# Kernel tuning notes

Hardware: AMD Instinct MI355X
Metric: run time of the kernel (lower is better)

Reference implementation:

```python
import jax, jax.numpy as jnp
import numpy as np

L, H, D, E, V, MAXS = 12, 12, 64, 768, 50257, 1024

def _ln(x, g, b, eps=1e-5):
    m = jnp.mean(x, axis=-1, keepdims=True)
    v = jnp.mean(jnp.square(x - m), axis=-1, keepdims=True)
    return (x - m) * jax.lax.rsqrt(v + eps) * g + b

def setup_inputs() -> dict:
    key = jax.random.key(0)
    ks = jax.random.split(key, 16)
    s = 0.02
    inp = {
        "input_ids": jax.random.randint(ks[0], (1, 1), 0, V),
        "past_key": jax.random.normal(ks[1], (L, 1, H, MAXS, D), jnp.float32),
        "past_value": jax.random.normal(ks[2], (L, 1, H, MAXS, D), jnp.float32),
        "past_seq_len": 1023,
        "attention_mask": jnp.ones((1, MAXS), jnp.float32),
        "wte": jax.random.normal(ks[3], (V, E), jnp.float32) * s,
        "wpe": jax.random.normal(ks[4], (MAXS, E), jnp.float32) * s,
        "ln1_g": jnp.ones((L, E), jnp.float32),
        "ln1_b": jnp.zeros((L, E), jnp.float32),
        "attn_w": jax.random.normal(ks[5], (L, E, 3 * E), jnp.float32) * s,
        "attn_b": jnp.zeros((L, 3 * E), jnp.float32),
        "proj_w": jax.random.normal(ks[6], (L, E, E), jnp.float32) * s,
        "proj_b": jnp.zeros((L, E), jnp.float32),
        "ln2_g": jnp.ones((L, E), jnp.float32),
        "ln2_b": jnp.zeros((L, E), jnp.float32),
        "fc_w": jax.random.normal(ks[7], (L, E, 4 * E), jnp.float32) * s,
        "fc_b": jnp.zeros((L, 4 * E), jnp.float32),
        "mlp_w": jax.random.normal(ks[8], (L, 4 * E, E), jnp.float32) * s,
        "mlp_b": jnp.zeros((L, E), jnp.float32),
        "lnf_g": jnp.ones((E,), jnp.float32),
        "lnf_b": jnp.zeros((E,), jnp.float32),
    }
    return inp

def reference(input_ids, past_key, past_value, past_seq_len, attention_mask,
              wte, wpe, ln1_g, ln1_b, attn_w, attn_b, proj_w, proj_b,
              ln2_g, ln2_b, fc_w, fc_b, mlp_w, mlp_b, lnf_g, lnf_b):
    S = int(past_seq_len)  # static cache length
    h = wte[input_ids] + wpe[S]                      # [1,1,E]
    bias = (1.0 - attention_mask[:, :S + 1]) * -1e9  # [1,S+1]
    scale = 1.0 / jnp.sqrt(jnp.float32(D))
    pk, pv = past_key, past_value
    for l in range(L):
        x = _ln(h, ln1_g[l], ln1_b[l])
        qkv = x @ attn_w[l] + attn_b[l]              # [1,1,3E]
        q, k, v = jnp.split(qkv, 3, axis=-1)
        q = q.reshape(1, 1, H, D).transpose(0, 2, 1, 3)  # [1,H,1,D]
        k = k.reshape(1, 1, H, D).transpose(0, 2, 1, 3)
        v = v.reshape(1, 1, H, D).transpose(0, 2, 1, 3)
        k_full = jnp.concatenate([pk[l, :, :, :S, :], k], axis=2)  # [1,H,S+1,D]
        v_full = jnp.concatenate([pv[l, :, :, :S, :], v], axis=2)
        scores = jnp.einsum('bhqd,bhkd->bhqk', q, k_full) * scale
        scores = scores + bias[:, None, None, :]
        attn = jax.nn.softmax(scores, axis=-1)
        o = jnp.einsum('bhqk,bhkd->bhqd', attn, v_full)
        o = o.transpose(0, 2, 1, 3).reshape(1, 1, H * D)
        h = h + o @ proj_w[l] + proj_b[l]
        x2 = _ln(h, ln2_g[l], ln2_b[l])
        h = h + jax.nn.gelu(x2 @ fc_w[l] + fc_b[l], approximate=True) @ mlp_w[l] + mlp_b[l]
        pk = pk.at[l, :, :, S, :].set(k[:, :, 0, :])
        pv = pv.at[l, :, :, S, :].set(v[:, :, 0, :])
    h = _ln(h, lnf_g, lnf_b)
    logits = h @ wte.T                               # [1,1,V] (tied lm_head)
    return (logits, pk, pv)
```

## Files before the change

kernel.cpp:

```cpp
#include <hip/hip_runtime.h>
#include <math.h>

#define EMB 768
#define NH 12
#define HD 64
#define NL 12
#define NV 50257
#define MAXS 1024
#define S_PAST 1023
#define E3 2304
#define E4 3072

#define WS_H    0
#define WS_QKV  768
#define WS_FC   3072
#define WS_PART 6144

__device__ __forceinline__ void blockReduce2(float& a, float& b, volatile float* ra, volatile float* rb) {
  int lane = threadIdx.x & 63, wid = threadIdx.x >> 6;
#pragma unroll
  for (int o = 32; o > 0; o >>= 1) { a += __shfl_down(a, o); b += __shfl_down(b, o); }
  if (lane == 0) { ra[wid] = a; rb[wid] = b; }
  __syncthreads();
  if (threadIdx.x == 0) {
    ra[0] = ra[0] + ra[1] + ra[2] + ra[3];
    rb[0] = rb[0] + rb[1] + rb[2] + rb[3];
  }
  __syncthreads();
  a = ra[0]; b = rb[0];
}

__global__ void copy_embed(const float* __restrict__ pk, const float* __restrict__ pv,
                           float* __restrict__ opk, float* __restrict__ opv,
                           const int* __restrict__ ids, const float* __restrict__ wte,
                           const float* __restrict__ wpe, const float* __restrict__ attn_b,
                           float* __restrict__ hvec, float* __restrict__ qkv) {
  int tid = threadIdx.x;
  if (blockIdx.x >= 2048) {
    int bi = blockIdx.x - 2048;
    qkv[bi * 256 + tid] = attn_b[bi * 256 + tid];
    if (bi < 3) {
      int id = ids[0];
      int e = bi * 256 + tid;
      hvec[e] = wte[(size_t)id * EMB + e] + wpe[(size_t)S_PAST * EMB + e];
    }
    return;
  }
  const size_t n4 = (size_t)NL * NH * MAXS * HD / 4;
  const float4* pk4 = (const float4*)pk;
  const float4* pv4 = (const float4*)pv;
  float4* opk4 = (float4*)opk;
  float4* opv4 = (float4*)opv;
  for (size_t i = (size_t)blockIdx.x * 256 + tid; i < n4; i += (size_t)2048 * 256) {
    opk4[i] = pk4[i];
    opv4[i] = pv4[i];
  }
}

template<int R>
__global__ void ln_gemv4(const float* __restrict__ hvec, const float* __restrict__ g,
                         const float* __restrict__ bb, const float* __restrict__ W,
                         float* __restrict__ out, int N, int l) {
  __shared__ float lh[EMB];
  __shared__ float xs[R];
  __shared__ float ra[4], rb[4];
  __shared__ float4 red[4][64];
  int tid = threadIdx.x, lane = tid & 63, wid = tid >> 6;
  float s1 = 0.f, s2 = 0.f;
  for (int e = tid; e < EMB; e += 256) { float v = hvec[e]; lh[e] = v; s1 += v; s2 += v * v; }
  blockReduce2(s1, s2, ra, rb);
  float mean = s1 * (1.f / EMB);
  float var = s2 * (1.f / EMB) - mean * mean;
  float rstd = rsqrtf(var + 1e-5f);
  int e0 = blockIdx.y * R;
  if (tid < R) {
    int e = e0 + tid;
    xs[tid] = (lh[e] - mean) * rstd * g[l * EMB + e] + bb[l * EMB + e];
  }
  __syncthreads();
  int j4 = blockIdx.x * 64 + lane;
  int N4 = N >> 2;
  const float4* p = (const float4*)(W + (size_t)l * EMB * N) + (size_t)e0 * N4 + j4 + (size_t)wid * N4;
  float4 w[R / 4];
#pragma unroll
  for (int i = 0; i < R / 4; i++) w[i] = p[(size_t)(i * 4) * N4];
  float4 acc = {0.f, 0.f, 0.f, 0.f};
#pragma unroll
  for (int i = 0; i < R / 4; i++) {
    float x = xs[wid + i * 4];
    acc.x += x * w[i].x; acc.y += x * w[i].y; acc.z += x * w[i].z; acc.w += x * w[i].w;
  }
  red[wid][lane] = acc;
  __syncthreads();
  if (wid == 0) {
    float4 a0 = red[0][lane], a1 = red[1][lane], a2 = red[2][lane], a3 = red[3][lane];
    float rx = a0.x + a1.x + a2.x + a3.x;
    float ry = a0.y + a1.y + a2.y + a3.y;
    float rz = a0.z + a1.z + a2.z + a3.z;
    float rw = a0.w + a1.w + a2.w + a3.w;
    float* op = out + (size_t)j4 * 4;
    atomicAdd(op + 0, rx); atomicAdd(op + 1, ry);
    atomicAdd(op + 2, rz); atomicAdd(op + 3, rw);
  }
}

__global__ void attn_kv(const float* __restrict__ qkv, const float* __restrict__ pk,
                        const float* __restrict__ pv, const float* __restrict__ mask,
                        float* __restrict__ opk, float* __restrict__ opv,
                        float* __restrict__ part, int l) {
  int h = blockIdx.x >> 4, c = blockIdx.x & 15;
  int tid = threadIdx.x, lane = tid & 63, wid = tid >> 6;
  int sub = tid & 15, grp = tid >> 4;
  __shared__ float4 qs4[16];
  __shared__ float sc[64];
  __shared__ float4 redo[4][16];
  if (tid < 16) qs4[tid] = ((const float4*)(qkv + h * 64))[tid];
  __syncthreads();
  size_t base = ((size_t)(l * NH + h) * MAXS) * HD;
  const float4* K4 = (const float4*)(pk + base);
  const float4* V4 = (const float4*)(pv + base);
  int t0 = c * 64;
  float4 kreg[4];
#pragma unroll
  for (int i = 0; i < 4; i++) {
    int t = t0 + grp + i * 16;
    kreg[i] = (t == S_PAST) ? ((const float4*)(qkv + EMB + h * 64))[sub] : K4[(size_t)t * 16 + sub];
  }
  if (c == 15 && grp == 15)
    ((float4*)(opk + base))[(size_t)S_PAST * 16 + sub] = kreg[3];
  float4 q4 = qs4[sub];
#pragma unroll
  for (int i = 0; i < 4; i++) {
    int key = grp + i * 16;
    float p = q4.x * kreg[i].x + q4.y * kreg[i].y + q4.z * kreg[i].z + q4.w * kreg[i].w;
    p += __shfl_xor(p, 1); p += __shfl_xor(p, 2);
    p += __shfl_xor(p, 4); p += __shfl_xor(p, 8);
    if (sub == 0) sc[key] = p * 0.125f + (1.f - mask[t0 + key]) * (-1e9f);
  }
  __syncthreads();
  if (wid == 0) {
    float a = sc[lane];
    float m = a;
#pragma unroll
    for (int o = 32; o > 0; o >>= 1) m = fmaxf(m, __shfl_down(m, o));
    m = __shfl(m, 0);
    float ea = expf(a - m);
    sc[lane] = ea;
    float s = ea;
#pragma unroll
    for (int o = 32; o > 0; o >>= 1) s += __shfl_down(s, o);
    if (lane == 0) { part[(h * 16 + c) * 68 + 0] = m; part[(h * 16 + c) * 68 + 1] = s; }
  }
  __syncthreads();
  float4 vreg[4];
#pragma unroll
  for (int i = 0; i < 4; i++) {
    int t = t0 + grp + i * 16;
    vreg[i] = (t == S_PAST) ? ((const float4*)(qkv + 2 * EMB + h * 64))[sub] : V4[(size_t)t * 16 + sub];
  }
  if (c == 15 && grp == 15)
    ((float4*)(opv + base))[(size_t)S_PAST * 16 + sub] = vreg[3];
  float4 acc = {0.f, 0.f, 0.f, 0.f};
#pragma unroll
  for (int i = 0; i < 4; i++) {
    float w = sc[grp + i * 16];
    acc.x += w * vreg[i].x; acc.y += w * vreg[i].y; acc.z += w * vreg[i].z; acc.w += w * vreg[i].w;
  }
  acc.x += __shfl_xor(acc.x, 16); acc.y += __shfl_xor(acc.y, 16);
  acc.z += __shfl_xor(acc.z, 16); acc.w += __shfl_xor(acc.w, 16);
  acc.x += __shfl_xor(acc.x, 32); acc.y += __shfl_xor(acc.y, 32);
  acc.z += __shfl_xor(acc.z, 32); acc.w += __shfl_xor(acc.w, 32);
  if (lane < 16) redo[wid][lane] = acc;
  __syncthreads();
  if (tid < 16) {
    float4 a0 = redo[0][tid], a1 = redo[1][tid], a2 = redo[2][tid], a3 = redo[3][tid];
    float4 r;
    r.x = a0.x + a1.x + a2.x + a3.x;
    r.y = a0.y + a1.y + a2.y + a3.y;
    r.z = a0.z + a1.z + a2.z + a3.z;
    r.w = a0.w + a1.w + a2.w + a3.w;
    ((float4*)(part + (h * 16 + c) * 68 + 4))[tid] = r;
  }
}

__global__ void proj_attn(const float* __restrict__ part, const float* __restrict__ W,
                          const float* __restrict__ bias, const float* __restrict__ fc_b,
                          float* __restrict__ hout, float* __restrict__ wfc, int l) {
  int jb = blockIdx.x;
  int rt = blockIdx.y;
  int h = rt >> 2, esub = rt & 3;
  int tid = threadIdx.x, lane = tid & 63, wid = tid >> 6;
  __shared__ float xs[16];
  __shared__ float4 red[4][64];
  if (tid < 16) {
    float M = -1e30f;
#pragma unroll
    for (int cc = 0; cc < 16; cc++) M = fmaxf(M, part[(h * 16 + cc) * 68]);
    float T = 0.f, o = 0.f;
    int d = esub * 16 + tid;
#pragma unroll
    for (int cc = 0; cc < 16; cc++) {
      float w = expf(part[(h * 16 + cc) * 68] - M);
      T += part[(h * 16 + cc) * 68 + 1] * w;
      o += part[(h * 16 + cc) * 68 + 4 + d] * w;
    }
    xs[tid] = o / T;
  }
  int bid = rt * 3 + jb;
  if (bid < 12) wfc[bid * 256 + tid] = fc_b[l * E4 + bid * 256 + tid];
  __syncthreads();
  int j4 = jb * 64 + lane;
  const int N4 = EMB >> 2;
  int r0 = h * 64 + esub * 16;
  const float4* p = (const float4*)(W + (size_t)l * EMB * EMB) + (size_t)(r0 + wid) * N4 + j4;
  float4 w[4];
#pragma unroll
  for (int i = 0; i < 4; i++) w[i] = p[(size_t)(i * 4) * N4];
  float4 acc = {0.f, 0.f, 0.f, 0.f};
#pragma unroll
  for (int i = 0; i < 4; i++) {
    float x = xs[wid + i * 4];
    acc.x += x * w[i].x; acc.y += x * w[i].y; acc.z += x * w[i].z; acc.w += x * w[i].w;
  }
  red[wid][lane] = acc;
  __syncthreads();
  if (wid == 0) {
    float4 a0 = red[0][lane], a1 = red[1][lane], a2 = red[2][lane], a3 = red[3][lane];
    float rx = a0.x + a1.x + a2.x + a3.x;
    float ry = a0.y + a1.y + a2.y + a3.y;
    float rz = a0.z + a1.z + a2.z + a3.z;
    float rw = a0.w + a1.w + a2.w + a3.w;
    if (rt == 0) {
      const float* bp = bias + l * EMB + jb * 256 + lane * 4;
      rx += bp[0]; ry += bp[1]; rz += bp[2]; rw += bp[3];
    }
    float* op = hout + (size_t)jb * 256 + (size_t)lane * 4;
    atomicAdd(op + 0, rx); atomicAdd(op + 1, ry);
    atomicAdd(op + 2, rz); atomicAdd(op + 3, rw);
  }
}

__global__ void mlp_gemv4(const float* __restrict__ fcv, const float* __restrict__ W,
                          const float* __restrict__ bias, const float* __restrict__ attn_b,
                          float* __restrict__ hout, float* __restrict__ qkv, int l) {
  __shared__ float xs[64];
  __shared__ float4 red[4][64];
  int tid = threadIdx.x, lane = tid & 63, wid = tid >> 6;
  int e0 = blockIdx.y * 64;
  if (tid < 64) {
    float x = fcv[e0 + tid];
    xs[tid] = 0.5f * x * (1.f + tanhf(0.7978845608028654f * (x + 0.044715f * x * x * x)));
  }
  int bid = blockIdx.y * 3 + blockIdx.x;
  if (l + 1 < NL && bid < 9) qkv[bid * 256 + tid] = attn_b[(l + 1) * E3 + bid * 256 + tid];
  __syncthreads();
  int j4 = blockIdx.x * 64 + lane;
  const int N4 = EMB >> 2;
  const float4* p = (const float4*)(W + (size_t)l * E4 * EMB) + (size_t)(e0 + wid) * N4 + j4;
  float4 w[16];
#pragma unroll
  for (int i = 0; i < 16; i++) w[i] = p[(size_t)(i * 4) * N4];
  float4 acc = {0.f, 0.f, 0.f, 0.f};
#pragma unroll
  for (int i = 0; i < 16; i++) {
    float x = xs[wid + i * 4];
    acc.x += x * w[i].x; acc.y += x * w[i].y; acc.z += x * w[i].z; acc.w += x * w[i].w;
  }
  red[wid][lane] = acc;
  __syncthreads();
  if (wid == 0) {
    float4 a0 = red[0][lane], a1 = red[1][lane], a2 = red[2][lane], a3 = red[3][lane];
    float rx = a0.x + a1.x + a2.x + a3.x;
    float ry = a0.y + a1.y + a2.y + a3.y;
    float rz = a0.z + a1.z + a2.z + a3.z;
    float rw = a0.w + a1.w + a2.w + a3.w;
    if (blockIdx.y == 0) {
      const float* bp = bias + l * EMB + j4 * 4;
      rx += bp[0]; ry += bp[1]; rz += bp[2]; rw += bp[3];
    }
    float* op = hout + (size_t)j4 * 4;
    atomicAdd(op + 0, rx); atomicAdd(op + 1, ry);
    atomicAdd(op + 2, rz); atomicAdd(op + 3, rw);
  }
}

__global__ void logits_lnf(const float* __restrict__ hvec, const float* __restrict__ g,
                           const float* __restrict__ b, const float* __restrict__ wte,
                           float* __restrict__ out) {
  __shared__ float4 xs4[192];
  __shared__ float ra[4], rb[4];
  int tid = threadIdx.x, lane = tid & 63, wid = tid >> 6;
  float s1 = 0.f, s2 = 0.f;
  float v0[3];
  int k = 0;
  for (int e = tid; e < EMB; e += 256, k++) { float v = hvec[e]; v0[k] = v; s1 += v; s2 += v * v; }
  blockReduce2(s1, s2, ra, rb);
  float mean = s1 * (1.f / EMB);
  float var = s2 * (1.f / EMB) - mean * mean;
  float rstd = rsqrtf(var + 1e-5f);
  k = 0;
  for (int e = tid; e < EMB; e += 256, k++)
    ((float*)xs4)[e] = (v0[k] - mean) * rstd * g[e] + b[e];
  __syncthreads();
  int v = blockIdx.x * 4 + wid;
  if (v >= NV) return;
  const float4* row = (const float4*)(wte + (size_t)v * EMB);
  float4 a0 = row[lane], a1 = row[lane + 64], a2 = row[lane + 128];
  float4 x0 = xs4[lane], x1 = xs4[lane + 64], x2 = xs4[lane + 128];
  float acc = a0.x * x0.x + a0.y * x0.y + a0.z * x0.z + a0.w * x0.w
            + a1.x * x1.x + a1.y * x1.y + a1.z * x1.z + a1.w * x1.w
            + a2.x * x2.x + a2.y * x2.y + a2.z * x2.z + a2.w * x2.w;
#pragma unroll
  for (int o = 32; o > 0; o >>= 1) acc += __shfl_down(acc, o);
  if (lane == 0) out[v] = acc;
}

extern "C" void kernel_launch(void* const* d_in, const int* in_sizes, int n_in,
                              void* d_out, int out_size, void* d_ws, size_t ws_size,
                              hipStream_t stream) {
  const int* input_ids = (const int*)d_in[0];
  const float* past_key = (const float*)d_in[1];
  const float* past_value = (const float*)d_in[2];
  const float* mask = (const float*)d_in[4];
  const float* wte = (const float*)d_in[5];
  const float* wpe = (const float*)d_in[6];
  const float* ln1_g = (const float*)d_in[7];
  const float* ln1_b = (const float*)d_in[8];
  const float* attn_w = (const float*)d_in[9];
  const float* attn_b = (const float*)d_in[10];
  const float* proj_w = (const float*)d_in[11];
  const float* proj_b = (const float*)d_in[12];
  const float* ln2_g = (const float*)d_in[13];
  const float* ln2_b = (const float*)d_in[14];
  const float* fc_w = (const float*)d_in[15];
  const float* fc_b = (const float*)d_in[16];
  const float* mlp_w = (const float*)d_in[17];
  const float* mlp_b = (const float*)d_in[18];
  const float* lnf_g = (const float*)d_in[19];
  const float* lnf_b = (const float*)d_in[20];

  float* out = (float*)d_out;
  float* out_logits = out;
  float* out_pk = out + NV;
  float* out_pv = out_pk + (size_t)NL * NH * MAXS * HD;

  float* ws = (float*)d_ws;
  float* wh = ws + WS_H;
  float* wqkv = ws + WS_QKV;
  float* wfc = ws + WS_FC;
  float* wpart = ws + WS_PART;

  copy_embed<<<2057, 256, 0, stream>>>(past_key, past_value, out_pk, out_pv,
                                       input_ids, wte, wpe, attn_b, wh, wqkv);

  for (int l = 0; l < NL; l++) {
    ln_gemv4<32><<<dim3(9, 24), 256, 0, stream>>>(wh, ln1_g, ln1_b, attn_w, wqkv, E3, l);
    attn_kv<<<192, 256, 0, stream>>>(wqkv, past_key, past_value, mask, out_pk, out_pv, wpart, l);
    proj_attn<<<dim3(3, 48), 256, 0, stream>>>(wpart, proj_w, proj_b, fc_b, wh, wfc, l);
    ln_gemv4<32><<<dim3(12, 24), 256, 0, stream>>>(wh, ln2_g, ln2_b, fc_w, wfc, E4, l);
    mlp_gemv4<<<dim3(3, 48), 256, 0, stream>>>(wfc, mlp_w, mlp_b, attn_b, wh, wqkv, l);
  }
  logits_lnf<<<12565, 256, 0, stream>>>(wh, lnf_g, lnf_b, wte, out_logits);
}
```

Before: 498.5 us.

## Fuse per-layer phases with in-kernel flag sync and overlap KV-cache copy in waits

Replaces five launches per layer with two kernels. Inside each kernel, blocks run different phases (QKV gemv, attention, projection, then FC and MLP) and order themselves with global atomic counters and release flags. The upfront bulk copy of the KV cache is removed. Blocks that are waiting on a flag instead take copy tiles from a shared atomic ticket, and the final logits kernel finishes any tiles that remain. The goals are to cut launch overhead and to hide the large cache copy behind dependent work. The risks are spin-wait deadlock if the waiting blocks are not co-resident with the producers, and extra atomic traffic.

```diff
diff --git a/kernel.cpp b/kernel.cpp
--- a/kernel.cpp
+++ b/kernel.cpp
@@ -11,10 +11,71 @@
 #define E3 2304
 #define E4 3072
 
-#define WS_H    0
-#define WS_QKV  768
-#define WS_FC   3072
-#define WS_PART 6144
+typedef unsigned int u32;
+
+#define KV_F4 2359296u
+#define TILE_F4 512u
+#define HALF_TILES 4608u
+#define NTILES 9216u
+
+#define WI_TICKET 0
+#define WI_CNT(l,k) (32 + ((l)*3 + (k)) * 16)
+#define WI_REL(l,k) (1024 + ((l)*3 + (k)) * 16)
+#define WF_H    2048
+#define WF_QKV  (WF_H + EMB)
+#define WF_FC   (WF_QKV + E3)
+#define WF_PART (WF_FC + E4)
+
+struct CopyCtx {
+  const float4* pk4; const float4* pv4;
+  float4* opk4; float4* opv4; u32* ticket;
+};
+
+__device__ __forceinline__ void copy_tile(const CopyCtx& cc, u32 t) {
+  bool isv = t >= HALF_TILES;
+  u32 tt = isv ? t - HALF_TILES : t;
+  const float4* src = isv ? cc.pv4 : cc.pk4;
+  float4* dst = isv ? cc.opv4 : cc.opk4;
+  u32 base = tt * TILE_F4 + threadIdx.x;
+#pragma unroll
+  for (int i = 0; i < 2; i++) {
+    u32 idx = base + i * 256;
+    u32 row = (idx >> 4) & (MAXS - 1);
+    float4 v = src[idx];
+    if (row != S_PAST) dst[idx] = v;
+  }
+}
+
+__device__ __forceinline__ void wait_rel(u32* rel, const CopyCtx& cc, u32* sscr) {
+  bool qdone = false;
+  while (true) {
+    if (threadIdx.x == 0)
+      sscr[0] = __hip_atomic_load(rel, __ATOMIC_ACQUIRE, __HIP_MEMORY_SCOPE_AGENT);
+    __syncthreads();
+    u32 f = sscr[0];
+    __syncthreads();
+    if (f) break;
+    if (!qdone) {
+      if (threadIdx.x == 0) sscr[1] = atomicAdd(cc.ticket, 1u);
+      __syncthreads();
+      u32 t = sscr[1];
+      __syncthreads();
+      if (t < NTILES) copy_tile(cc, t); else qdone = true;
+    } else {
+      __builtin_amdgcn_s_sleep(8);
+    }
+  }
+}
+
+__device__ __forceinline__ void signal(u32* cnt, u32* rel, u32 n) {
+  __syncthreads();
+  __threadfence();
+  if (threadIdx.x == 0) {
+    u32 old = atomicAdd(cnt, 1u);
+    if (old == n - 1)
+      __hip_atomic_store(rel, 1u, __ATOMIC_RELEASE, __HIP_MEMORY_SCOPE_AGENT);
+  }
+}
 
 __device__ __forceinline__ void blockReduce2(float& a, float& b, volatile float* ra, volatile float* rb) {
   int lane = threadIdx.x & 63, wid = threadIdx.x >> 6;
@@ -30,41 +91,19 @@
   a = ra[0]; b = rb[0];
 }
 
-__global__ void copy_embed(const float* __restrict__ pk, const float* __restrict__ pv,
-                           float* __restrict__ opk, float* __restrict__ opv,
-                           const int* __restrict__ ids, const float* __restrict__ wte,
-                           const float* __restrict__ wpe, const float* __restrict__ attn_b,
-                           float* __restrict__ hvec, float* __restrict__ qkv) {
-  int tid = threadIdx.x;
-  if (blockIdx.x >= 2048) {
-    int bi = blockIdx.x - 2048;
-    qkv[bi * 256 + tid] = attn_b[bi * 256 + tid];
-    if (bi < 3) {
-      int id = ids[0];
-      int e = bi * 256 + tid;
-      hvec[e] = wte[(size_t)id * EMB + e] + wpe[(size_t)S_PAST * EMB + e];
-    }
-    return;
-  }
-  const size_t n4 = (size_t)NL * NH * MAXS * HD / 4;
-  const float4* pk4 = (const float4*)pk;
-  const float4* pv4 = (const float4*)pv;
-  float4* opk4 = (float4*)opk;
-  float4* opv4 = (float4*)opv;
-  for (size_t i = (size_t)blockIdx.x * 256 + tid; i < n4; i += (size_t)2048 * 256) {
-    opk4[i] = pk4[i];
-    opv4[i] = pv4[i];
-  }
-}
-
-template<int R>
-__global__ void ln_gemv4(const float* __restrict__ hvec, const float* __restrict__ g,
-                         const float* __restrict__ bb, const float* __restrict__ W,
-                         float* __restrict__ out, int N, int l) {
-  __shared__ float lh[EMB];
-  __shared__ float xs[R];
-  __shared__ float ra[4], rb[4];
-  __shared__ float4 red[4][64];
+__device__ __forceinline__ float gelu(float x) {
+  return 0.5f * x * (1.f + tanhf(0.7978845608028654f * (x + 0.044715f * x * x * x)));
+}
+
+__device__ void phase_ln_gemv48(int et, int jt, const float* __restrict__ hvec,
+                                const float* __restrict__ g, const float* __restrict__ bb,
+                                const float* __restrict__ W, float* __restrict__ out,
+                                int N, int l, float* smem) {
+  float* lh = smem;
+  float* xs = smem + 768;
+  volatile float* ra = smem + 816;
+  volatile float* rb = smem + 820;
+  float4* red = (float4*)(smem + 832);
   int tid = threadIdx.x, lane = tid & 63, wid = tid >> 6;
   float s1 = 0.f, s2 = 0.f;
   for (int e = tid; e < EMB; e += 256) { float v = hvec[e]; lh[e] = v; s1 += v; s2 += v * v; }
@@ -72,28 +111,28 @@
   float mean = s1 * (1.f / EMB);
   float var = s2 * (1.f / EMB) - mean * mean;
   float rstd = rsqrtf(var + 1e-5f);
-  int e0 = blockIdx.y * R;
-  if (tid < R) {
+  int e0 = et * 48;
+  if (tid < 48) {
     int e = e0 + tid;
     xs[tid] = (lh[e] - mean) * rstd * g[l * EMB + e] + bb[l * EMB + e];
   }
   __syncthreads();
-  int j4 = blockIdx.x * 64 + lane;
+  int j4 = jt * 64 + lane;
   int N4 = N >> 2;
-  const float4* p = (const float4*)(W + (size_t)l * EMB * N) + (size_t)e0 * N4 + j4 + (size_t)wid * N4;
-  float4 w[R / 4];
-#pragma unroll
-  for (int i = 0; i < R / 4; i++) w[i] = p[(size_t)(i * 4) * N4];
+  const float4* p = (const float4*)(W + (size_t)l * EMB * N) + (size_t)(e0 + wid) * N4 + j4;
+  float4 w[12];
+#pragma unroll
+  for (int i = 0; i < 12; i++) w[i] = p[(size_t)(i * 4) * N4];
   float4 acc = {0.f, 0.f, 0.f, 0.f};
 #pragma unroll
-  for (int i = 0; i < R / 4; i++) {
+  for (int i = 0; i < 12; i++) {
     float x = xs[wid + i * 4];
     acc.x += x * w[i].x; acc.y += x * w[i].y; acc.z += x * w[i].z; acc.w += x * w[i].w;
   }
-  red[wid][lane] = acc;
+  red[wid * 64 + lane] = acc;
   __syncthreads();
   if (wid == 0) {
-    float4 a0 = red[0][lane], a1 = red[1][lane], a2 = red[2][lane], a3 = red[3][lane];
+    float4 a0 = red[lane], a1 = red[64 + lane], a2 = red[128 + lane], a3 = red[192 + lane];
     float rx = a0.x + a1.x + a2.x + a3.x;
     float ry = a0.y + a1.y + a2.y + a3.y;
     float rz = a0.z + a1.z + a2.z + a3.z;
@@ -104,16 +143,16 @@
   }
 }
 
-__global__ void attn_kv(const float* __restrict__ qkv, const float* __restrict__ pk,
-                        const float* __restrict__ pv, const float* __restrict__ mask,
-                        float* __restrict__ opk, float* __restrict__ opv,
-                        float* __restrict__ part, int l) {
-  int h = blockIdx.x >> 4, c = blockIdx.x & 15;
+__device__ void phase_attn(int h, int c, const float* __restrict__ qkv,
+                           const float* __restrict__ pk, const float* __restrict__ pv,
+                           const float* __restrict__ mask, float* __restrict__ opk,
+                           float* __restrict__ opv, float* __restrict__ part,
+                           int l, float* smem) {
+  float4* qs4 = (float4*)smem;
+  float* sc = smem + 64;
+  float4* redo = (float4*)(smem + 128);
   int tid = threadIdx.x, lane = tid & 63, wid = tid >> 6;
   int sub = tid & 15, grp = tid >> 4;
-  __shared__ float4 qs4[16];
-  __shared__ float sc[64];
-  __shared__ float4 redo[4][16];
   if (tid < 16) qs4[tid] = ((const float4*)(qkv + h * 64))[tid];
   __syncthreads();
   size_t base = ((size_t)(l * NH + h) * MAXS) * HD;
@@ -170,10 +209,10 @@
   acc.z += __shfl_xor(acc.z, 16); acc.w += __shfl_xor(acc.w, 16);
   acc.x += __shfl_xor(acc.x, 32); acc.y += __shfl_xor(acc.y, 32);
   acc.z += __shfl_xor(acc.z, 32); acc.w += __shfl_xor(acc.w, 32);
-  if (lane < 16) redo[wid][lane] = acc;
+  if (lane < 16) redo[wid * 16 + lane] = acc;
   __syncthreads();
   if (tid < 16) {
-    float4 a0 = redo[0][tid], a1 = redo[1][tid], a2 = redo[2][tid], a3 = redo[3][tid];
+    float4 a0 = redo[tid], a1 = redo[16 + tid], a2 = redo[32 + tid], a3 = redo[48 + tid];
     float4 r;
     r.x = a0.x + a1.x + a2.x + a3.x;
     r.y = a0.y + a1.y + a2.y + a3.y;
@@ -183,31 +222,27 @@
   }
 }
 
-__global__ void proj_attn(const float* __restrict__ part, const float* __restrict__ W,
-                          const float* __restrict__ bias, const float* __restrict__ fc_b,
-                          float* __restrict__ hout, float* __restrict__ wfc, int l) {
-  int jb = blockIdx.x;
-  int rt = blockIdx.y;
+__device__ void phase_proj(int rt, int jb, const float* __restrict__ part,
+                           const float* __restrict__ W, const float* __restrict__ bias,
+                           float* __restrict__ hout, int l, float* smem) {
   int h = rt >> 2, esub = rt & 3;
+  float* xs = smem;
+  float4* red = (float4*)(smem + 16);
   int tid = threadIdx.x, lane = tid & 63, wid = tid >> 6;
-  __shared__ float xs[16];
-  __shared__ float4 red[4][64];
   if (tid < 16) {
     float M = -1e30f;
 #pragma unroll
-    for (int cc = 0; cc < 16; cc++) M = fmaxf(M, part[(h * 16 + cc) * 68]);
+    for (int q = 0; q < 16; q++) M = fmaxf(M, part[(h * 16 + q) * 68]);
     float T = 0.f, o = 0.f;
     int d = esub * 16 + tid;
 #pragma unroll
-    for (int cc = 0; cc < 16; cc++) {
-      float w = expf(part[(h * 16 + cc) * 68] - M);
-      T += part[(h * 16 + cc) * 68 + 1] * w;
-      o += part[(h * 16 + cc) * 68 + 4 + d] * w;
+    for (int q = 0; q < 16; q++) {
+      float w = expf(part[(h * 16 + q) * 68] - M);
+      T += part[(h * 16 + q) * 68 + 1] * w;
+      o += part[(h * 16 + q) * 68 + 4 + d] * w;
     }
     xs[tid] = o / T;
   }
-  int bid = rt * 3 + jb;
-  if (bid < 12) wfc[bid * 256 + tid] = fc_b[l * E4 + bid * 256 + tid];
   __syncthreads();
   int j4 = jb * 64 + lane;
   const int N4 = EMB >> 2;
@@ -222,10 +257,10 @@
     float x = xs[wid + i * 4];
     acc.x += x * w[i].x; acc.y += x * w[i].y; acc.z += x * w[i].z; acc.w += x * w[i].w;
   }
-  red[wid][lane] = acc;
+  red[wid * 64 + lane] = acc;
   __syncthreads();
   if (wid == 0) {
-    float4 a0 = red[0][lane], a1 = red[1][lane], a2 = red[2][lane], a3 = red[3][lane];
+    float4 a0 = red[lane], a1 = red[64 + lane], a2 = red[128 + lane], a3 = red[192 + lane];
     float rx = a0.x + a1.x + a2.x + a3.x;
     float ry = a0.y + a1.y + a2.y + a3.y;
     float rz = a0.z + a1.z + a2.z + a3.z;
@@ -240,21 +275,16 @@
   }
 }
 
-__global__ void mlp_gemv4(const float* __restrict__ fcv, const float* __restrict__ W,
-                          const float* __restrict__ bias, const float* __restrict__ attn_b,
-                          float* __restrict__ hout, float* __restrict__ qkv, int l) {
-  __shared__ float xs[64];
-  __shared__ float4 red[4][64];
+__device__ void phase_mlp(int etile, int jb, const float* __restrict__ fcv,
+                          const float* __restrict__ W, const float* __restrict__ bias,
+                          float* __restrict__ hout, int l, float* smem) {
+  float* xs = smem;
+  float4* red = (float4*)(smem + 64);
   int tid = threadIdx.x, lane = tid & 63, wid = tid >> 6;
-  int e0 = blockIdx.y * 64;
-  if (tid < 64) {
-    float x = fcv[e0 + tid];
-    xs[tid] = 0.5f * x * (1.f + tanhf(0.7978845608028654f * (x + 0.044715f * x * x * x)));
-  }
-  int bid = blockIdx.y * 3 + blockIdx.x;
-  if (l + 1 < NL && bid < 9) qkv[bid * 256 + tid] = attn_b[(l + 1) * E3 + bid * 256 + tid];
-  __syncthreads();
-  int j4 = blockIdx.x * 64 + lane;
+  int e0 = etile * 64;
+  if (tid < 64) xs[tid] = gelu(fcv[e0 + tid]);
+  __syncthreads();
+  int j4 = jb * 64 + lane;
   const int N4 = EMB >> 2;
   const float4* p = (const float4*)(W + (size_t)l * E4 * EMB) + (size_t)(e0 + wid) * N4 + j4;
   float4 w[16];
@@ -266,15 +296,15 @@
     float x = xs[wid + i * 4];
     acc.x += x * w[i].x; acc.y += x * w[i].y; acc.z += x * w[i].z; acc.w += x * w[i].w;
   }
-  red[wid][lane] = acc;
+  red[wid * 64 + lane] = acc;
   __syncthreads();
   if (wid == 0) {
-    float4 a0 = red[0][lane], a1 = red[1][lane], a2 = red[2][lane], a3 = red[3][lane];
+    float4 a0 = red[lane], a1 = red[64 + lane], a2 = red[128 + lane], a3 = red[192 + lane];
     float rx = a0.x + a1.x + a2.x + a3.x;
     float ry = a0.y + a1.y + a2.y + a3.y;
     float rz = a0.z + a1.z + a2.z + a3.z;
     float rw = a0.w + a1.w + a2.w + a3.w;
-    if (blockIdx.y == 0) {
+    if (etile == 0) {
       const float* bp = bias + l * EMB + j4 * 4;
       rx += bp[0]; ry += bp[1]; rz += bp[2]; rw += bp[3];
     }
@@ -284,11 +314,93 @@
   }
 }
 
-__global__ void logits_lnf(const float* __restrict__ hvec, const float* __restrict__ g,
-                           const float* __restrict__ b, const float* __restrict__ wte,
-                           float* __restrict__ out) {
-  __shared__ float4 xs4[192];
+__global__ __launch_bounds__(256) void init_kernel(
+    const int* __restrict__ ids, const float* __restrict__ wte,
+    const float* __restrict__ wpe, const float* __restrict__ attn_b,
+    float* __restrict__ wsf) {
+  int idx = blockIdx.x * 256 + threadIdx.x;
+  float* h = wsf + WF_H;
+  float* qkv = wsf + WF_QKV;
+  if (idx < E3) qkv[idx] = attn_b[idx];
+  if (idx < EMB) {
+    int id = ids[0];
+    h[idx] = wte[(size_t)id * EMB + idx] + wpe[(size_t)S_PAST * EMB + idx];
+  }
+}
+
+__global__ __launch_bounds__(256) void k1_qkv_attn_proj(
+    const float* __restrict__ pk, const float* __restrict__ pv,
+    const float* __restrict__ mask,
+    const float* __restrict__ ln1_g, const float* __restrict__ ln1_b,
+    const float* __restrict__ attn_w, const float* __restrict__ proj_w,
+    const float* __restrict__ proj_b, const float* __restrict__ fc_b,
+    float* __restrict__ opk, float* __restrict__ opv,
+    float* __restrict__ wsf, int l) {
+  __shared__ __align__(16) float smem[1856];
+  __shared__ u32 sscr[2];
+  u32* wsu = (u32*)wsf;
+  float* wh = wsf + WF_H;
+  float* wqkv = wsf + WF_QKV;
+  float* wfc = wsf + WF_FC;
+  float* wpart = wsf + WF_PART;
+  CopyCtx cc = {(const float4*)pk, (const float4*)pv, (float4*)opk, (float4*)opv, wsu + WI_TICKET};
+  int bi = blockIdx.x, tid = threadIdx.x;
+  if (bi < 144) {
+    phase_ln_gemv48(bi / 9, bi % 9, wh, ln1_g, ln1_b, attn_w, wqkv, E3, l, smem);
+    signal(wsu + WI_CNT(l, 0), wsu + WI_REL(l, 0), 144);
+    wait_rel(wsu + WI_REL(l, 1), cc, sscr);
+  } else if (bi < 336) {
+    wait_rel(wsu + WI_REL(l, 0), cc, sscr);
+    int ai = bi - 144;
+    phase_attn(ai >> 4, ai & 15, wqkv, pk, pv, mask, opk, opv, wpart, l, smem);
+    signal(wsu + WI_CNT(l, 1), wsu + WI_REL(l, 1), 192);
+  } else {
+    int pi = bi - 336;
+    if (pi < 12) wfc[pi * 256 + tid] = fc_b[l * E4 + pi * 256 + tid];
+    wait_rel(wsu + WI_REL(l, 1), cc, sscr);
+    phase_proj(pi / 3, pi % 3, wpart, proj_w, proj_b, wh, l, smem);
+  }
+}
+
+__global__ __launch_bounds__(256) void k2_fc_mlp(
+    const float* __restrict__ pk, const float* __restrict__ pv,
+    const float* __restrict__ ln2_g, const float* __restrict__ ln2_b,
+    const float* __restrict__ fc_w, const float* __restrict__ mlp_w,
+    const float* __restrict__ mlp_b, const float* __restrict__ attn_b,
+    float* __restrict__ opk, float* __restrict__ opv,
+    float* __restrict__ wsf, int l) {
+  __shared__ __align__(16) float smem[1856];
+  __shared__ u32 sscr[2];
+  u32* wsu = (u32*)wsf;
+  float* wh = wsf + WF_H;
+  float* wqkv = wsf + WF_QKV;
+  float* wfc = wsf + WF_FC;
+  CopyCtx cc = {(const float4*)pk, (const float4*)pv, (float4*)opk, (float4*)opv, wsu + WI_TICKET};
+  int bi = blockIdx.x, tid = threadIdx.x;
+  if (bi < 192) {
+    phase_ln_gemv48(bi / 12, bi % 12, wh, ln2_g, ln2_b, fc_w, wfc, E4, l, smem);
+    signal(wsu + WI_CNT(l, 2), wsu + WI_REL(l, 2), 192);
+  } else {
+    int ei = bi - 192;
+    if (l + 1 < NL && ei < 9)
+      wqkv[ei * 256 + tid] = attn_b[(l + 1) * E3 + ei * 256 + tid];
+    wait_rel(wsu + WI_REL(l, 2), cc, sscr);
+    phase_mlp(ei / 3, ei % 3, wfc, mlp_w, mlp_b, wh, l, smem);
+  }
+}
+
+__global__ __launch_bounds__(256) void logits_lnf_drain(
+    const float* __restrict__ g, const float* __restrict__ b,
+    const float* __restrict__ wte, float* __restrict__ out,
+    const float* __restrict__ pk, const float* __restrict__ pv,
+    float* __restrict__ opk, float* __restrict__ opv,
+    float* __restrict__ wsf) {
+  __shared__ __align__(16) float4 xs4[192];
   __shared__ float ra[4], rb[4];
+  __shared__ u32 sscr[2];
+  u32* wsu = (u32*)wsf;
+  const float* hvec = wsf + WF_H;
+  CopyCtx cc = {(const float4*)pk, (const float4*)pv, (float4*)opk, (float4*)opv, wsu + WI_TICKET};
   int tid = threadIdx.x, lane = tid & 63, wid = tid >> 6;
   float s1 = 0.f, s2 = 0.f;
   float v0[3];
@@ -303,16 +415,29 @@
     ((float*)xs4)[e] = (v0[k] - mean) * rstd * g[e] + b[e];
   __syncthreads();
   int v = blockIdx.x * 4 + wid;
-  if (v >= NV) return;
-  const float4* row = (const float4*)(wte + (size_t)v * EMB);
-  float4 a0 = row[lane], a1 = row[lane + 64], a2 = row[lane + 128];
-  float4 x0 = xs4[lane], x1 = xs4[lane + 64], x2 = xs4[lane + 128];
-  float acc = a0.x * x0.x + a0.y * x0.y + a0.z * x0.z + a0.w * x0.w
-            + a1.x * x1.x + a1.y * x1.y + a1.z * x1.z + a1.w * x1.w
-            + a2.x * x2.x + a2.y * x2.y + a2.z * x2.z + a2.w * x2.w;
-#pragma unroll
-  for (int o = 32; o > 0; o >>= 1) acc += __shfl_down(acc, o);
-  if (lane == 0) out[v] = acc;
+  if (v < NV) {
+    const float4* row = (const float4*)(wte + (size_t)v * EMB);
+    float4 a0 = row[lane], a1 = row[lane + 64], a2 = row[lane + 128];
+    float4 x0 = xs4[lane], x1 = xs4[lane + 64], x2 = xs4[lane + 128];
+    float acc = a0.x * x0.x + a0.y * x0.y + a0.z * x0.z + a0.w * x0.w
+              + a1.x * x1.x + a1.y * x1.y + a1.z * x1.z + a1.w * x1.w
+              + a2.x * x2.x + a2.y * x2.y + a2.z * x2.z + a2.w * x2.w;
+#pragma unroll
+    for (int o = 32; o > 0; o >>= 1) acc += __shfl_down(acc, o);
+    if (lane == 0) out[v] = acc;
+  }
+  if (tid == 0) sscr[0] = __hip_atomic_load(cc.ticket, __ATOMIC_RELAXED, __HIP_MEMORY_SCOPE_AGENT);
+  __syncthreads();
+  if (sscr[0] < NTILES) {
+    bool qdone = false;
+    while (!qdone) {
+      if (tid == 0) sscr[1] = atomicAdd(cc.ticket, 1u);
+      __syncthreads();
+      u32 t = sscr[1];
+      __syncthreads();
+      if (t < NTILES) copy_tile(cc, t); else qdone = true;
+    }
+  }
 }
 
 extern "C" void kernel_launch(void* const* d_in, const int* in_sizes, int n_in,
@@ -343,22 +468,17 @@
   float* out_logits = out;
   float* out_pk = out + NV;
   float* out_pv = out_pk + (size_t)NL * NH * MAXS * HD;
-
-  float* ws = (float*)d_ws;
-  float* wh = ws + WS_H;
-  float* wqkv = ws + WS_QKV;
-  float* wfc = ws + WS_FC;
-  float* wpart = ws + WS_PART;
-
-  copy_embed<<<2057, 256, 0, stream>>>(past_key, past_value, out_pk, out_pv,
-                                       input_ids, wte, wpe, attn_b, wh, wqkv);
+  float* wsf = (float*)d_ws;
+
+  hipMemsetAsync(d_ws, 0, 8192, stream);
+  init_kernel<<<9, 256, 0, stream>>>(input_ids, wte, wpe, attn_b, wsf);
 
   for (int l = 0; l < NL; l++) {
-    ln_gemv4<32><<<dim3(9, 24), 256, 0, stream>>>(wh, ln1_g, ln1_b, attn_w, wqkv, E3, l);
-    attn_kv<<<192, 256, 0, stream>>>(wqkv, past_key, past_value, mask, out_pk, out_pv, wpart, l);
-    proj_attn<<<dim3(3, 48), 256, 0, stream>>>(wpart, proj_w, proj_b, fc_b, wh, wfc, l);
-    ln_gemv4<32><<<dim3(12, 24), 256, 0, stream>>>(wh, ln2_g, ln2_b, fc_w, wfc, E4, l);
-    mlp_gemv4<<<dim3(3, 48), 256, 0, stream>>>(wfc, mlp_w, mlp_b, attn_b, wh, wqkv, l);
-  }
-  logits_lnf<<<12565, 256, 0, stream>>>(wh, lnf_g, lnf_b, wte, out_logits);
-}
+    k1_qkv_attn_proj<<<480, 256, 0, stream>>>(past_key, past_value, mask,
+        ln1_g, ln1_b, attn_w, proj_w, proj_b, fc_b, out_pk, out_pv, wsf, l);
+    k2_fc_mlp<<<336, 256, 0, stream>>>(past_key, past_value,
+        ln2_g, ln2_b, fc_w, mlp_w, mlp_b, attn_b, out_pk, out_pv, wsf, l);
+  }
+  logits_lnf_drain<<<12565, 256, 0, stream>>>(lnf_g, lnf_b, wte, out_logits,
+      past_key, past_value, out_pk, out_pv, wsf);
+}
```

Measured after the change: 1.693 ms. 3.4x slower.

## Fuse KV-cache copy into attention kernel and hoist weight loads before reductions

Applied to the files above, without the earlier changes.

Removes the standalone full KV-cache copy kernel and has the per-layer attention kernel write every K/V row it already loads in registers to the output cache. This avoids reading the past cache twice from memory. Separately, weight loads in the GEMV, projection, MLP and logits kernels are issued before the layernorm/softmax-merge reductions and barriers to overlap memory latency with those computations. The attention kernels now carry additional store traffic and register pressure.

```diff
diff --git a/kernel.cpp b/kernel.cpp
--- a/kernel.cpp
+++ b/kernel.cpp
@@ -30,63 +30,47 @@
   a = ra[0]; b = rb[0];
 }
 
-__global__ void copy_embed(const float* __restrict__ pk, const float* __restrict__ pv,
-                           float* __restrict__ opk, float* __restrict__ opv,
-                           const int* __restrict__ ids, const float* __restrict__ wte,
-                           const float* __restrict__ wpe, const float* __restrict__ attn_b,
-                           float* __restrict__ hvec, float* __restrict__ qkv) {
-  int tid = threadIdx.x;
-  if (blockIdx.x >= 2048) {
-    int bi = blockIdx.x - 2048;
-    qkv[bi * 256 + tid] = attn_b[bi * 256 + tid];
-    if (bi < 3) {
-      int id = ids[0];
-      int e = bi * 256 + tid;
-      hvec[e] = wte[(size_t)id * EMB + e] + wpe[(size_t)S_PAST * EMB + e];
-    }
-    return;
-  }
-  const size_t n4 = (size_t)NL * NH * MAXS * HD / 4;
-  const float4* pk4 = (const float4*)pk;
-  const float4* pv4 = (const float4*)pv;
-  float4* opk4 = (float4*)opk;
-  float4* opv4 = (float4*)opv;
-  for (size_t i = (size_t)blockIdx.x * 256 + tid; i < n4; i += (size_t)2048 * 256) {
-    opk4[i] = pk4[i];
-    opv4[i] = pv4[i];
-  }
-}
-
-template<int R>
+__global__ void init_kernel(const int* __restrict__ ids, const float* __restrict__ wte,
+                            const float* __restrict__ wpe, const float* __restrict__ attn_b,
+                            float* __restrict__ hvec, float* __restrict__ qkv) {
+  int idx = blockIdx.x * 256 + threadIdx.x;
+  if (idx < E3) qkv[idx] = attn_b[idx];
+  if (idx < EMB) {
+    int id = ids[0];
+    hvec[idx] = wte[(size_t)id * EMB + idx] + wpe[(size_t)S_PAST * EMB + idx];
+  }
+}
+
 __global__ void ln_gemv4(const float* __restrict__ hvec, const float* __restrict__ g,
                          const float* __restrict__ bb, const float* __restrict__ W,
                          float* __restrict__ out, int N, int l) {
   __shared__ float lh[EMB];
-  __shared__ float xs[R];
+  __shared__ float xs[32];
   __shared__ float ra[4], rb[4];
   __shared__ float4 red[4][64];
   int tid = threadIdx.x, lane = tid & 63, wid = tid >> 6;
-  float s1 = 0.f, s2 = 0.f;
-  for (int e = tid; e < EMB; e += 256) { float v = hvec[e]; lh[e] = v; s1 += v; s2 += v * v; }
+  int e0 = blockIdx.y * 32;
+  float hv0 = hvec[tid], hv1 = hvec[tid + 256], hv2 = hvec[tid + 512];
+  int j4 = blockIdx.x * 64 + lane;
+  int N4 = N >> 2;
+  const float4* p = (const float4*)(W + (size_t)l * EMB * N) + (size_t)(e0 + wid) * N4 + j4;
+  float4 w[8];
+#pragma unroll
+  for (int i = 0; i < 8; i++) w[i] = p[(size_t)(i * 4) * N4];
+  float gv = 0.f, bv = 0.f;
+  if (tid < 32) { gv = g[l * EMB + e0 + tid]; bv = bb[l * EMB + e0 + tid]; }
+  lh[tid] = hv0; lh[tid + 256] = hv1; lh[tid + 512] = hv2;
+  float s1 = hv0 + hv1 + hv2;
+  float s2 = hv0 * hv0 + hv1 * hv1 + hv2 * hv2;
   blockReduce2(s1, s2, ra, rb);
   float mean = s1 * (1.f / EMB);
   float var = s2 * (1.f / EMB) - mean * mean;
   float rstd = rsqrtf(var + 1e-5f);
-  int e0 = blockIdx.y * R;
-  if (tid < R) {
-    int e = e0 + tid;
-    xs[tid] = (lh[e] - mean) * rstd * g[l * EMB + e] + bb[l * EMB + e];
-  }
-  __syncthreads();
-  int j4 = blockIdx.x * 64 + lane;
-  int N4 = N >> 2;
-  const float4* p = (const float4*)(W + (size_t)l * EMB * N) + (size_t)e0 * N4 + j4 + (size_t)wid * N4;
-  float4 w[R / 4];
-#pragma unroll
-  for (int i = 0; i < R / 4; i++) w[i] = p[(size_t)(i * 4) * N4];
+  if (tid < 32) xs[tid] = (lh[e0 + tid] - mean) * rstd * gv + bv;
+  __syncthreads();
   float4 acc = {0.f, 0.f, 0.f, 0.f};
 #pragma unroll
-  for (int i = 0; i < R / 4; i++) {
+  for (int i = 0; i < 8; i++) {
     float x = xs[wid + i * 4];
     acc.x += x * w[i].x; acc.y += x * w[i].y; acc.z += x * w[i].z; acc.w += x * w[i].w;
   }
@@ -119,6 +103,8 @@
   size_t base = ((size_t)(l * NH + h) * MAXS) * HD;
   const float4* K4 = (const float4*)(pk + base);
   const float4* V4 = (const float4*)(pv + base);
+  float4* oK4 = (float4*)(opk + base);
+  float4* oV4 = (float4*)(opv + base);
   int t0 = c * 64;
   float4 kreg[4];
 #pragma unroll
@@ -126,8 +112,11 @@
     int t = t0 + grp + i * 16;
     kreg[i] = (t == S_PAST) ? ((const float4*)(qkv + EMB + h * 64))[sub] : K4[(size_t)t * 16 + sub];
   }
-  if (c == 15 && grp == 15)
-    ((float4*)(opk + base))[(size_t)S_PAST * 16 + sub] = kreg[3];
+#pragma unroll
+  for (int i = 0; i < 4; i++) {
+    int t = t0 + grp + i * 16;
+    oK4[(size_t)t * 16 + sub] = kreg[i];
+  }
   float4 q4 = qs4[sub];
 #pragma unroll
   for (int i = 0; i < 4; i++) {
@@ -158,8 +147,11 @@
     int t = t0 + grp + i * 16;
     vreg[i] = (t == S_PAST) ? ((const float4*)(qkv + 2 * EMB + h * 64))[sub] : V4[(size_t)t * 16 + sub];
   }
-  if (c == 15 && grp == 15)
-    ((float4*)(opv + base))[(size_t)S_PAST * 16 + sub] = vreg[3];
+#pragma unroll
+  for (int i = 0; i < 4; i++) {
+    int t = t0 + grp + i * 16;
+    oV4[(size_t)t * 16 + sub] = vreg[i];
+  }
   float4 acc = {0.f, 0.f, 0.f, 0.f};
 #pragma unroll
   for (int i = 0; i < 4; i++) {
@@ -192,23 +184,6 @@
   int tid = threadIdx.x, lane = tid & 63, wid = tid >> 6;
   __shared__ float xs[16];
   __shared__ float4 red[4][64];
-  if (tid < 16) {
-    float M = -1e30f;
-#pragma unroll
-    for (int cc = 0; cc < 16; cc++) M = fmaxf(M, part[(h * 16 + cc) * 68]);
-    float T = 0.f, o = 0.f;
-    int d = esub * 16 + tid;
-#pragma unroll
-    for (int cc = 0; cc < 16; cc++) {
-      float w = expf(part[(h * 16 + cc) * 68] - M);
-      T += part[(h * 16 + cc) * 68 + 1] * w;
-      o += part[(h * 16 + cc) * 68 + 4 + d] * w;
-    }
-    xs[tid] = o / T;
-  }
-  int bid = rt * 3 + jb;
-  if (bid < 12) wfc[bid * 256 + tid] = fc_b[l * E4 + bid * 256 + tid];
-  __syncthreads();
   int j4 = jb * 64 + lane;
   const int N4 = EMB >> 2;
   int r0 = h * 64 + esub * 16;
@@ -216,6 +191,23 @@
   float4 w[4];
 #pragma unroll
   for (int i = 0; i < 4; i++) w[i] = p[(size_t)(i * 4) * N4];
+  if (tid < 16) {
+    float M = -1e30f;
+#pragma unroll
+    for (int q = 0; q < 16; q++) M = fmaxf(M, part[(h * 16 + q) * 68]);
+    float T = 0.f, o = 0.f;
+    int d = esub * 16 + tid;
+#pragma unroll
+    for (int q = 0; q < 16; q++) {
+      float wq = expf(part[(h * 16 + q) * 68] - M);
+      T += part[(h * 16 + q) * 68 + 1] * wq;
+      o += part[(h * 16 + q) * 68 + 4 + d] * wq;
+    }
+    xs[tid] = o / T;
+  }
+  int bid = rt * 3 + jb;
+  if (bid < 12) wfc[bid * 256 + tid] = fc_b[l * E4 + bid * 256 + tid];
+  __syncthreads();
   float4 acc = {0.f, 0.f, 0.f, 0.f};
 #pragma unroll
   for (int i = 0; i < 4; i++) {
@@ -247,19 +239,19 @@
   __shared__ float4 red[4][64];
   int tid = threadIdx.x, lane = tid & 63, wid = tid >> 6;
   int e0 = blockIdx.y * 64;
-  if (tid < 64) {
-    float x = fcv[e0 + tid];
-    xs[tid] = 0.5f * x * (1.f + tanhf(0.7978845608028654f * (x + 0.044715f * x * x * x)));
-  }
-  int bid = blockIdx.y * 3 + blockIdx.x;
-  if (l + 1 < NL && bid < 9) qkv[bid * 256 + tid] = attn_b[(l + 1) * E3 + bid * 256 + tid];
-  __syncthreads();
   int j4 = blockIdx.x * 64 + lane;
   const int N4 = EMB >> 2;
   const float4* p = (const float4*)(W + (size_t)l * E4 * EMB) + (size_t)(e0 + wid) * N4 + j4;
   float4 w[16];
 #pragma unroll
   for (int i = 0; i < 16; i++) w[i] = p[(size_t)(i * 4) * N4];
+  if (tid < 64) {
+    float x = fcv[e0 + tid];
+    xs[tid] = 0.5f * x * (1.f + tanhf(0.7978845608028654f * (x + 0.044715f * x * x * x)));
+  }
+  int bid = blockIdx.y * 3 + blockIdx.x;
+  if (l + 1 < NL && bid < 9) qkv[bid * 256 + tid] = attn_b[(l + 1) * E3 + bid * 256 + tid];
+  __syncthreads();
   float4 acc = {0.f, 0.f, 0.f, 0.f};
 #pragma unroll
   for (int i = 0; i < 16; i++) {
@@ -290,22 +282,24 @@
   __shared__ float4 xs4[192];
   __shared__ float ra[4], rb[4];
   int tid = threadIdx.x, lane = tid & 63, wid = tid >> 6;
-  float s1 = 0.f, s2 = 0.f;
-  float v0[3];
-  int k = 0;
-  for (int e = tid; e < EMB; e += 256, k++) { float v = hvec[e]; v0[k] = v; s1 += v; s2 += v * v; }
+  float hv0 = hvec[tid], hv1 = hvec[tid + 256], hv2 = hvec[tid + 512];
+  int v = blockIdx.x * 4 + wid;
+  float4 a0 = {0,0,0,0}, a1 = {0,0,0,0}, a2 = {0,0,0,0};
+  if (v < NV) {
+    const float4* row = (const float4*)(wte + (size_t)v * EMB);
+    a0 = row[lane]; a1 = row[lane + 64]; a2 = row[lane + 128];
+  }
+  float s1 = hv0 + hv1 + hv2;
+  float s2 = hv0 * hv0 + hv1 * hv1 + hv2 * hv2;
   blockReduce2(s1, s2, ra, rb);
   float mean = s1 * (1.f / EMB);
   float var = s2 * (1.f / EMB) - mean * mean;
   float rstd = rsqrtf(var + 1e-5f);
-  k = 0;
-  for (int e = tid; e < EMB; e += 256, k++)
-    ((float*)xs4)[e] = (v0[k] - mean) * rstd * g[e] + b[e];
-  __syncthreads();
-  int v = blockIdx.x * 4 + wid;
+  ((float*)xs4)[tid]       = (hv0 - mean) * rstd * g[tid]       + b[tid];
+  ((float*)xs4)[tid + 256] = (hv1 - mean) * rstd * g[tid + 256] + b[tid + 256];
+  ((float*)xs4)[tid + 512] = (hv2 - mean) * rstd * g[tid + 512] + b[tid + 512];
+  __syncthreads();
   if (v >= NV) return;
-  const float4* row = (const float4*)(wte + (size_t)v * EMB);
-  float4 a0 = row[lane], a1 = row[lane + 64], a2 = row[lane + 128];
   float4 x0 = xs4[lane], x1 = xs4[lane + 64], x2 = xs4[lane + 128];
   float acc = a0.x * x0.x + a0.y * x0.y + a0.z * x0.z + a0.w * x0.w
             + a1.x * x1.x + a1.y * x1.y + a1.z * x1.z + a1.w * x1.w
@@ -350,14 +344,13 @@
   float* wfc = ws + WS_FC;
   float* wpart = ws + WS_PART;
 
-  copy_embed<<<2057, 256, 0, stream>>>(past_key, past_value, out_pk, out_pv,
-                                       input_ids, wte, wpe, attn_b, wh, wqkv);
+  init_kernel<<<9, 256, 0, stream>>>(input_ids, wte, wpe, attn_b, wh, wqkv);
 
   for (int l = 0; l < NL; l++) {
-    ln_gemv4<32><<<dim3(9, 24), 256, 0, stream>>>(wh, ln1_g, ln1_b, attn_w, wqkv, E3, l);
+    ln_gemv4<<<dim3(9, 24), 256, 0, stream>>>(wh, ln1_g, ln1_b, attn_w, wqkv, E3, l);
     attn_kv<<<192, 256, 0, stream>>>(wqkv, past_key, past_value, mask, out_pk, out_pv, wpart, l);
     proj_attn<<<dim3(3, 48), 256, 0, stream>>>(wpart, proj_w, proj_b, fc_b, wh, wfc, l);
-    ln_gemv4<32><<<dim3(12, 24), 256, 0, stream>>>(wh, ln2_g, ln2_b, fc_w, wfc, E4, l);
+    ln_gemv4<<<dim3(12, 24), 256, 0, stream>>>(wh, ln2_g, ln2_b, fc_w, wfc, E4, l);
     mlp_gemv4<<<dim3(3, 48), 256, 0, stream>>>(wfc, mlp_w, mlp_b, attn_b, wh, wqkv, l);
   }
   logits_lnf<<<12565, 256, 0, stream>>>(wh, lnf_g, lnf_b, wte, out_logits);
```

Measured after the change: 448.5 us. 1.11x faster.
